# Kernel optimization log

Measured on AMD Instinct MI355X. Metric: run time of the kernel, lower is better.

## Reference

```python
import jax, jax.numpy as jnp
import numpy as np

T_HORIZON, S_DIM, A_DIM, H = 65536, 128, 8, 256
GAMMA, LMBDA, EPS_CLIP, VF_COEF, ENT_COEF = 0.99, 0.95, 0.2, 0.5, 0.01
LOG2PI = float(np.log(2.0 * np.pi))


def setup_inputs() -> dict:
    key = jax.random.key(0)
    ks = jax.random.split(key, 24)
    s = jax.random.normal(ks[0], (T_HORIZON, S_DIM), jnp.float32)
    a = jax.random.normal(ks[1], (T_HORIZON, A_DIM), jnp.float32)
    r = jax.random.normal(ks[2], (T_HORIZON, 1), jnp.float32)
    sp = jax.random.normal(ks[3], (T_HORIZON, S_DIM), jnp.float32)
    log_prob_a_old = jax.random.normal(ks[4], (T_HORIZON, 1), jnp.float32)
    d_mask = (jax.random.uniform(ks[5], (T_HORIZON, 1)) > 0.05).astype(jnp.float32)

    def lin(k, fan_in, fan_out, std):
        return jax.random.normal(k, (fan_in, fan_out), jnp.float32) * (std / np.sqrt(fan_in))

    params = dict(
        pi_W1=lin(ks[6], S_DIM, H, np.sqrt(2)), pi_b1=jnp.zeros((H,), jnp.float32),
        pi_W2=lin(ks[7], H, H, np.sqrt(2)),     pi_b2=jnp.zeros((H,), jnp.float32),
        mu_W=lin(ks[8], H, A_DIM, 0.01),        mu_b=jnp.zeros((A_DIM,), jnp.float32),
        log_std=jnp.zeros((A_DIM,), jnp.float32),
        v_W1=lin(ks[9], S_DIM, H, np.sqrt(2)),  v_b1=jnp.zeros((H,), jnp.float32),
        v_W2=lin(ks[10], H, H, np.sqrt(2)),     v_b2=jnp.zeros((H,), jnp.float32),
        vh_W=lin(ks[11], H, 1, 1.0),            vh_b=jnp.zeros((1,), jnp.float32),
    )
    return dict(s=s, a=a, r=r, sp=sp, log_prob_a_old=log_prob_a_old, d_mask=d_mask, **params)


def reference(s, a, r, sp, log_prob_a_old, d_mask,
              pi_W1, pi_b1, pi_W2, pi_b2, mu_W, mu_b, log_std,
              v_W1, v_b1, v_W2, v_b2, vh_W, vh_b):
    def mlp(x, W1, b1, W2, b2):
        return jnp.tanh(jnp.tanh(x @ W1 + b1) @ W2 + b2)

    def v_fn(x):
        return mlp(x, v_W1, v_b1, v_W2, v_b2) @ vh_W + vh_b  # [N, 1]

    # ---- GAE (computed under no_grad in the original) ----
    values = jax.lax.stop_gradient(v_fn(s))                  # [T, 1]
    v_last = jax.lax.stop_gradient(v_fn(sp[-1:]))            # [1, 1]
    next_values = jnp.concatenate([values[1:], v_last], axis=0)
    deltas = r + GAMMA * next_values * d_mask - values       # [T, 1]

    def gae_step(gae, inp):
        delta, m = inp
        gae = delta + GAMMA * LMBDA * m * gae
        return gae, gae

    _, advantages = jax.lax.scan(gae_step, jnp.zeros((1,), deltas.dtype),
                                 (deltas, d_mask), reverse=True)  # [T, 1]
    returns = advantages + values
    advantages = (advantages - advantages.mean()) / (advantages.std(ddof=1) + 1e-8)
    advantages = jax.lax.stop_gradient(advantages)
    returns = jax.lax.stop_gradient(returns)

    # ---- PPO clipped loss (single full-batch pass) ----
    mu = mlp(s, pi_W1, pi_b1, pi_W2, pi_b2) @ mu_W + mu_b    # [T, A]
    std = jnp.exp(log_std)
    log_prob = (-0.5 * ((a - mu) / std) ** 2 - log_std - 0.5 * LOG2PI).sum(-1, keepdims=True)
    ratio = jnp.exp(log_prob - log_prob_a_old)               # [T, 1]
    pg_loss = -jnp.minimum(ratio * advantages,
                           jnp.clip(ratio, 1.0 - EPS_CLIP, 1.0 + EPS_CLIP) * advantages).mean()
    diff = v_fn(s) - returns
    vf_loss = jnp.where(jnp.abs(diff) < 1.0, 0.5 * diff ** 2, jnp.abs(diff) - 0.5).mean()
    entropy = (0.5 + 0.5 * LOG2PI + log_std).mean()          # Normal entropy, constant over batch
    return pg_loss + VF_COEF * vf_loss - ENT_COEF * entropy
```

## Files before the change

kernel.cpp:

```cpp
#include <hip/hip_runtime.h>
#include <math.h>

#define TH 65536
#define SD 128
#define AD 8
#define HD 256

constexpr float GAMMA  = 0.99f;
constexpr float LMBDA  = 0.95f;
constexpr float EPSC   = 0.2f;
constexpr float VFC    = 0.5f;
constexpr float ENTC   = 0.01f;
constexpr float LOG2PI = 1.8378770664093453f;

typedef _Float16 half8 __attribute__((ext_vector_type(8)));
typedef __fp16 fp16x2 __attribute__((ext_vector_type(2)));
typedef __attribute__((ext_vector_type(4))) float f32x4;

constexpr size_t WS_VALUES = 0;
constexpr size_t WS_RATIO  = 131080;
constexpr size_t WS_CHP    = 196616;
constexpr size_t WS_CHB    = 196680;
constexpr size_t WS_SCAL   = 196744;
constexpr size_t WS_BF     = 196752;
constexpr size_t SW_PIW1 = 0;
constexpr size_t SW_PIW2 = 32768;
constexpr size_t SW_VW1  = 98304;
constexpr size_t SW_VW2  = 131072;
constexpr size_t WS_S1P  = 295056;
constexpr size_t WS_S2P  = 295120;
constexpr size_t WS_VFP  = 295184;
constexpr size_t WS_PGP  = 295248;

__device__ __forceinline__ unsigned pk2h(float a, float b) {
    fp16x2 h = __builtin_amdgcn_cvt_pkrtz(a, b);
    return __builtin_bit_cast(unsigned, h);
}

__device__ __forceinline__ float ftanh(float x) {
    float e = __expf(x + x);
    return fmaf(-2.f, __builtin_amdgcn_rcpf(e + 1.f), 1.f);
}

__device__ __forceinline__ float atomLoad(const float* p) {
    return __hip_atomic_load(p, __ATOMIC_RELAXED, __HIP_MEMORY_SCOPE_AGENT);
}

__global__ __launch_bounds__(256) void swizzle_kernel(
    const float* __restrict__ piW1, const float* __restrict__ vW1,
    const float* __restrict__ piW2, const float* __restrict__ vW2,
    unsigned short* __restrict__ dPiW1, unsigned short* __restrict__ dVW1,
    unsigned short* __restrict__ dPiW2, unsigned short* __restrict__ dVW2,
    float* __restrict__ scal)
{
    if (blockIdx.x == 0 && threadIdx.x < 8) scal[threadIdx.x] = 0.f;
    int g = blockIdx.x * 256 + threadIdx.x;
    const float* S; unsigned short* D; int lo;
    if      (g <  8192) { S = piW1; D = dPiW1; lo = 0;     }
    else if (g < 24576) { S = piW2; D = dPiW2; lo = 8192;  }
    else if (g < 32768) { S = vW1;  D = dVW1;  lo = 24576; }
    else                { S = vW2;  D = dVW2;  lo = 32768; }
    int q = g - lo;
    int k = q >> 6, n4 = (q & 63) * 4;
    float4 v = *(const float4*)(S + (size_t)k * HD + n4);
    int ks = k >> 5, kq = (k >> 3) & 3, j = k & 7;
    int nt = n4 >> 4, nr = n4 & 15;
    unsigned short* base = D + ((size_t)(ks * 16 + nt) * 64 + kq * 16 + nr) * 8 + j;
    unsigned p01 = pk2h(v.x, v.y);
    unsigned p23 = pk2h(v.z, v.w);
    base[0]  = (unsigned short)(p01 & 0xffff);
    base[8]  = (unsigned short)(p01 >> 16);
    base[16] = (unsigned short)(p23 & 0xffff);
    base[24] = (unsigned short)(p23 >> 16);
}

__device__ __forceinline__ void runlayer1(
    f32x4* acc, const unsigned short* __restrict__ Ws,
    const half8* afr, int colhalf, int lane)
{
    const half8* Wp = (const half8*)Ws + (size_t)(colhalf * 8) * 64 + lane;
    half8 b[2][8];
#pragma unroll
    for (int nt = 0; nt < 8; ++nt) acc[nt] = (f32x4){0.f, 0.f, 0.f, 0.f};
#pragma unroll
    for (int nt = 0; nt < 8; ++nt) b[0][nt] = Wp[(0 * 16 + nt) * 64];
#pragma unroll
    for (int nt = 0; nt < 8; ++nt) b[1][nt] = Wp[(1 * 16 + nt) * 64];
#pragma unroll
    for (int ks = 0; ks < 4; ++ks) {
        const int cur = ks & 1;
#pragma unroll
        for (int nt = 0; nt < 8; ++nt)
            acc[nt] = __builtin_amdgcn_mfma_f32_16x16x32_f16(afr[ks], b[cur][nt], acc[nt], 0, 0, 0);
        if (ks < 2) {
#pragma unroll
            for (int nt = 0; nt < 8; ++nt) b[cur][nt] = Wp[((ks + 2) * 16 + nt) * 64];
        }
    }
}

__device__ __forceinline__ void runlayer2(
    f32x4* acc, const unsigned short* __restrict__ Ws,
    const unsigned short* h1, int l15, int quad, int rowgrp, int colhalf, int lane)
{
    const half8* Wp = (const half8*)Ws + (size_t)(colhalf * 8) * 64 + lane;
    const unsigned short* Ap = h1 + (rowgrp * 16 + l15) * 264 + quad * 8;
    half8 b[2][8];
    half8 af[2];
#pragma unroll
    for (int nt = 0; nt < 8; ++nt) acc[nt] = (f32x4){0.f, 0.f, 0.f, 0.f};
    af[0] = *(const half8*)(Ap + 0 * 32);
#pragma unroll
    for (int nt = 0; nt < 8; ++nt) b[0][nt] = Wp[(0 * 16 + nt) * 64];
    af[1] = *(const half8*)(Ap + 1 * 32);
#pragma unroll
    for (int nt = 0; nt < 8; ++nt) b[1][nt] = Wp[(1 * 16 + nt) * 64];
#pragma unroll
    for (int ks = 0; ks < 8; ++ks) {
        const int cur = ks & 1;
#pragma unroll
        for (int nt = 0; nt < 8; ++nt)
            acc[nt] = __builtin_amdgcn_mfma_f32_16x16x32_f16(af[cur], b[cur][nt], acc[nt], 0, 0, 0);
        if (ks < 6) {
            af[cur] = *(const half8*)(Ap + (ks + 2) * 32);
#pragma unroll
            for (int nt = 0; nt < 8; ++nt) b[cur][nt] = Wp[((ks + 2) * 16 + nt) * 64];
        }
    }
}

__device__ __forceinline__ void store4(unsigned short* dst, int stride,
                                       float t0, float t1, float t2, float t3)
{
    unsigned p01 = pk2h(t0, t1), p23 = pk2h(t2, t3);
    dst[0]          = (unsigned short)(p01 & 0xffff);
    dst[stride]     = (unsigned short)(p01 >> 16);
    dst[2 * stride] = (unsigned short)(p23 & 0xffff);
    dst[3 * stride] = (unsigned short)(p23 >> 16);
}

__global__ __launch_bounds__(256, 3) void mlp_fused_kernel(
    const float* __restrict__ X, const float* __restrict__ Xlast,
    const unsigned short* __restrict__ piW1s, const float* __restrict__ pib1,
    const unsigned short* __restrict__ piW2s, const float* __restrict__ pib2,
    const float* __restrict__ muW, const float* __restrict__ mub,
    const float* __restrict__ logstd,
    const float* __restrict__ act, const float* __restrict__ lpold,
    const unsigned short* __restrict__ vW1s, const float* __restrict__ vb1,
    const unsigned short* __restrict__ vW2s, const float* __restrict__ vb2,
    const float* __restrict__ vhW, const float* __restrict__ vhb,
    float* __restrict__ values, float* __restrict__ ratio)
{
    __shared__ unsigned short h1[32 * 264];
    __shared__ float cmb[32 * 8];
    __shared__ float val[32];
    const int tid = threadIdx.x;
    const int lane = tid & 63, wave = tid >> 6;
    const int l15 = lane & 15, quad = lane >> 4;
    const int rowgrp = wave >> 1, colhalf = wave & 1;
    const bool vonly = (blockIdx.x == gridDim.x - 1);
    const float* Xp = vonly ? Xlast : X + (size_t)blockIdx.x * 32 * SD;
    const int nrows = vonly ? 1 : 32;
    const int vout0 = vonly ? TH : blockIdx.x * 32;

    if (tid < 32) val[tid] = 0.f;
    cmb[tid] = 0.f;

    const int rr = rowgrp * 16 + l15;
    const float* xrow = Xp + (size_t)(rr < nrows ? rr : 0) * SD;
    half8 afr[4];
#pragma unroll
    for (int ks = 0; ks < 4; ++ks) {
        float4 v0 = *(const float4*)(xrow + ks * 32 + quad * 8);
        float4 v1 = *(const float4*)(xrow + ks * 32 + quad * 8 + 4);
        if (rr >= nrows) { v0 = make_float4(0.f, 0.f, 0.f, 0.f); v1 = v0; }
        uint4 u = make_uint4(pk2h(v0.x, v0.y), pk2h(v0.z, v0.w),
                             pk2h(v1.x, v1.y), pk2h(v1.z, v1.w));
        afr[ks] = __builtin_bit_cast(half8, u);
    }

    f32x4 acc[8];

    if (!vonly) {
        runlayer1(acc, piW1s, afr, colhalf, lane);
#pragma unroll
        for (int ntl = 0; ntl < 8; ++ntl) {
            int col = (colhalf * 8 + ntl) * 16 + l15;
            float bb = pib1[col];
            store4(&h1[(rowgrp * 16 + quad * 4) * 264 + col], 264,
                   ftanh(acc[ntl][0] + bb), ftanh(acc[ntl][1] + bb),
                   ftanh(acc[ntl][2] + bb), ftanh(acc[ntl][3] + bb));
        }
        __syncthreads();
        runlayer2(acc, piW2s, h1, l15, quad, rowgrp, colhalf, lane);
        float pm[4][8];
#pragma unroll
        for (int rg = 0; rg < 4; ++rg)
#pragma unroll
            for (int aj = 0; aj < 8; ++aj) pm[rg][aj] = 0.f;
#pragma unroll
        for (int ntl = 0; ntl < 8; ++ntl) {
            int col = (colhalf * 8 + ntl) * 16 + l15;
            float bb = pib2[col];
            float4 w0 = *(const float4*)(muW + (size_t)col * AD);
            float4 w1 = *(const float4*)(muW + (size_t)col * AD + 4);
            float wv[8] = {w0.x, w0.y, w0.z, w0.w, w1.x, w1.y, w1.z, w1.w};
#pragma unroll
            for (int rg = 0; rg < 4; ++rg) {
                float hv = ftanh(acc[ntl][rg] + bb);
#pragma unroll
                for (int aj = 0; aj < 8; ++aj) pm[rg][aj] = fmaf(hv, wv[aj], pm[rg][aj]);
            }
        }
#pragma unroll
        for (int off = 8; off >= 1; off >>= 1)
#pragma unroll
            for (int rg = 0; rg < 4; ++rg)
#pragma unroll
                for (int aj = 0; aj < 8; ++aj)
                    pm[rg][aj] += __shfl_xor(pm[rg][aj], off, 16);
        if (l15 == 0) {
#pragma unroll
            for (int rg = 0; rg < 4; ++rg) {
                int rowi = rowgrp * 16 + quad * 4 + rg;
#pragma unroll
                for (int aj = 0; aj < 8; ++aj)
                    atomicAdd(&cmb[rowi * 8 + aj], pm[rg][aj]);
            }
        }
        __syncthreads();
        if (tid < 32) {
            int row = blockIdx.x * 32 + tid;
            const float* ar = act + (size_t)row * AD;
            float lp = 0.f;
#pragma unroll
            for (int aj = 0; aj < 8; ++aj) {
                float ls = logstd[aj];
                float mu = cmb[tid * 8 + aj] + mub[aj];
                float z = (ar[aj] - mu) * __expf(-ls);
                lp += -0.5f * z * z - ls;
            }
            lp -= 4.f * LOG2PI;
            ratio[row] = __expf(lp - lpold[row]);
        }
        __syncthreads();
    }

    runlayer1(acc, vW1s, afr, colhalf, lane);
#pragma unroll
    for (int ntl = 0; ntl < 8; ++ntl) {
        int col = (colhalf * 8 + ntl) * 16 + l15;
        float bb = vb1[col];
        store4(&h1[(rowgrp * 16 + quad * 4) * 264 + col], 264,
               ftanh(acc[ntl][0] + bb), ftanh(acc[ntl][1] + bb),
               ftanh(acc[ntl][2] + bb), ftanh(acc[ntl][3] + bb));
    }
    __syncthreads();
    runlayer2(acc, vW2s, h1, l15, quad, rowgrp, colhalf, lane);
    float vp[4] = {0.f, 0.f, 0.f, 0.f};
#pragma unroll
    for (int ntl = 0; ntl < 8; ++ntl) {
        int col = (colhalf * 8 + ntl) * 16 + l15;
        float bb = vb2[col], w = vhW[col];
#pragma unroll
        for (int rg = 0; rg < 4; ++rg) vp[rg] += ftanh(acc[ntl][rg] + bb) * w;
    }
#pragma unroll
    for (int off = 8; off >= 1; off >>= 1)
#pragma unroll
        for (int rg = 0; rg < 4; ++rg) vp[rg] += __shfl_xor(vp[rg], off, 16);
    if (l15 == 0) {
#pragma unroll
        for (int rg = 0; rg < 4; ++rg)
            atomicAdd(&val[rowgrp * 16 + quad * 4 + rg], vp[rg]);
    }
    __syncthreads();
    if (tid < nrows)
        values[vout0 + tid] = val[tid] + vhb[0];
}

__device__ __forceinline__ void gae_block_scan(
    const float* __restrict__ rw, const float* __restrict__ m,
    const float* __restrict__ values, int t0, int j,
    float* sp_, float* sb_, float* ds, float* ms)
{
    float4 vv = *(const float4*)(values + t0);
    float v4 = values[t0 + 4];
    float4 rr = *(const float4*)(rw + t0);
    float4 mm = *(const float4*)(m + t0);
    float vs[5] = {vv.x, vv.y, vv.z, vv.w, v4};
    float rs[4] = {rr.x, rr.y, rr.z, rr.w};
    ms[0] = mm.x; ms[1] = mm.y; ms[2] = mm.z; ms[3] = mm.w;
    const float g = GAMMA * LMBDA;
#pragma unroll
    for (int i = 0; i < 4; ++i)
        ds[i] = rs[i] + GAMMA * vs[i + 1] * ms[i] - vs[i];

    float P = 1.f, B = 0.f;
#pragma unroll
    for (int i = 3; i >= 0; --i) {
        float p = g * ms[i];
        B = ds[i] + p * B;
        P = p * P;
    }
    sp_[j] = P; sb_[j] = B;
    __syncthreads();
    for (int dstep = 1; dstep < 256; dstep <<= 1) {
        float pj = sp_[j], bj = sb_[j], pk = 1.f, bk = 0.f;
        if (j + dstep < 256) { pk = sp_[j + dstep]; bk = sb_[j + dstep]; }
        __syncthreads();
        sp_[j] = pj * pk;
        sb_[j] = bj + pj * bk;
        __syncthreads();
    }
}

__device__ __forceinline__ float gae_carry(
    const float* __restrict__ chunkP, const float* __restrict__ chunkB,
    int j, int bid, float* cp, float* cb, float* bcast)
{
    if (j < 64) { cp[j] = chunkP[j]; cb[j] = chunkB[j]; }
    __syncthreads();
    if (j == 0) {
        float A = 0.f;
        for (int c = 63; c > bid; --c) A = cb[c] + cp[c] * A;
        bcast[0] = A;
    }
    __syncthreads();
    return bcast[0];
}

__global__ __launch_bounds__(256) void gae_scan_kernel(
    const float* __restrict__ rw, const float* __restrict__ m,
    const float* __restrict__ values,
    float* __restrict__ chunkP, float* __restrict__ chunkB)
{
    __shared__ float sp_[256], sb_[256];
    const int j = threadIdx.x;
    float ds[4], ms[4];
    gae_block_scan(rw, m, values, blockIdx.x * 1024 + j * 4, j, sp_, sb_, ds, ms);
    if (j == 0) { chunkP[blockIdx.x] = sp_[0]; chunkB[blockIdx.x] = sb_[0]; }
}

__global__ __launch_bounds__(256) void gae_mid_kernel(
    const float* __restrict__ rw, const float* __restrict__ m,
    const float* __restrict__ values,
    const float* __restrict__ chunkP, const float* __restrict__ chunkB,
    float* __restrict__ s1p, float* __restrict__ s2p, float* __restrict__ vfp)
{
    __shared__ float sp_[256], sb_[256];
    __shared__ float cp[64], cb[64];
    __shared__ float red[12];
    __shared__ float bcast[1];
    const int j = threadIdx.x;
    const float g = GAMMA * LMBDA;
    float ds[4], ms[4];
    gae_block_scan(rw, m, values, blockIdx.x * 1024 + j * 4, j, sp_, sb_, ds, ms);
    const float carry = gae_carry(chunkP, chunkB, j, blockIdx.x, cp, cb, bcast);

    float Pe = 1.f, Be = 0.f;
    if (j < 255) { Pe = sp_[j + 1]; Be = sb_[j + 1]; }
    float A = Be + Pe * carry;
    float s1 = 0.f, s2 = 0.f, vf = 0.f;
#pragma unroll
    for (int i = 3; i >= 0; --i) {
        A = ds[i] + g * ms[i] * A;
        float ab = fabsf(A);
        vf += (ab < 1.f) ? 0.5f * A * A : ab - 0.5f;
        s1 += A;
        s2 += A * A;
    }
#pragma unroll
    for (int off = 32; off >= 1; off >>= 1) {
        s1 += __shfl_down(s1, off, 64);
        s2 += __shfl_down(s2, off, 64);
        vf += __shfl_down(vf, off, 64);
    }
    if ((j & 63) == 0) {
        int w = j >> 6;
        red[w] = s1; red[4 + w] = s2; red[8 + w] = vf;
    }
    __syncthreads();
    if (j == 0) {
        s1p[blockIdx.x] = red[0] + red[1] + red[2] + red[3];
        s2p[blockIdx.x] = red[4] + red[5] + red[6] + red[7];
        vfp[blockIdx.x] = red[8] + red[9] + red[10] + red[11];
    }
}

__global__ __launch_bounds__(256) void gae_fin_kernel(
    const float* __restrict__ rw, const float* __restrict__ m,
    const float* __restrict__ values, const float* __restrict__ ratio,
    const float* __restrict__ logstd,
    const float* __restrict__ chunkP, const float* __restrict__ chunkB,
    const float* __restrict__ s1p, const float* __restrict__ s2p,
    const float* __restrict__ vfp,
    float* __restrict__ pgp, float* __restrict__ scal, float* __restrict__ out)
{
    __shared__ float sp_[256], sb_[256];
    __shared__ float cp[64], cb[64];
    __shared__ float red[4];
    __shared__ float bcast[4];
    const int j = threadIdx.x;
    const int t0 = blockIdx.x * 1024 + j * 4;
    const float g = GAMMA * LMBDA;
    float ds[4], ms[4];
    gae_block_scan(rw, m, values, t0, j, sp_, sb_, ds, ms);
    const float carry = gae_carry(chunkP, chunkB, j, blockIdx.x, cp, cb, bcast);

    if (j < 64) {
        float a = s1p[j], b = s2p[j], c = vfp[j];
#pragma unroll
        for (int off = 32; off >= 1; off >>= 1) {
            a += __shfl_down(a, off, 64);
            b += __shfl_down(b, off, 64);
            c += __shfl_down(c, off, 64);
        }
        if (j == 0) { bcast[1] = a; bcast[2] = b; bcast[3] = c; }
    }
    __syncthreads();
    const float ssum = bcast[1], ssq = bcast[2], vfs = bcast[3];
    const float meanA = ssum / (float)TH;
    const float varA = fmaxf((ssq - ssum * ssum / (float)TH) / (float)(TH - 1), 0.f);
    const float inv = 1.f / (sqrtf(varA) + 1e-8f);

    float Pe = 1.f, Be = 0.f;
    if (j < 255) { Pe = sp_[j + 1]; Be = sb_[j + 1]; }
    float A = Be + Pe * carry;
    float a4[4];
#pragma unroll
    for (int i = 3; i >= 0; --i) {
        A = ds[i] + g * ms[i] * A;
        a4[i] = A;
    }

    float4 r4 = *(const float4*)(ratio + t0);
    float rt[4] = {r4.x, r4.y, r4.z, r4.w};
    float pg = 0.f;
#pragma unroll
    for (int i = 0; i < 4; ++i) {
        float aN = (a4[i] - meanA) * inv;
        float rc = fminf(fmaxf(rt[i], 1.f - EPSC), 1.f + EPSC);
        pg -= fminf(rt[i] * aN, rc * aN);
    }
#pragma unroll
    for (int off = 32; off >= 1; off >>= 1) pg += __shfl_down(pg, off, 64);
    if ((j & 63) == 0) red[j >> 6] = pg;
    __syncthreads();
    if (j == 0) {
        pgp[blockIdx.x] = red[0] + red[1] + red[2] + red[3];
        __threadfence();
        float old = atomicAdd(&scal[4], 1.f);
        if (old == 63.f) {
            float pgs = 0.f;
            for (int c = 0; c < 64; ++c) pgs += atomLoad(&pgp[c]);
            float ls = 0.f;
#pragma unroll
            for (int jj = 0; jj < AD; ++jj) ls += logstd[jj];
            float entropy = 0.5f + 0.5f * LOG2PI + ls / (float)AD;
            out[0] = pgs / (float)TH + VFC * (vfs / (float)TH) - ENTC * entropy;
        }
    }
}

extern "C" void kernel_launch(void* const* d_in, const int* in_sizes, int n_in,
                              void* d_out, int out_size, void* d_ws, size_t ws_size,
                              hipStream_t stream) {
    const float* s      = (const float*)d_in[0];
    const float* a      = (const float*)d_in[1];
    const float* r      = (const float*)d_in[2];
    const float* sp     = (const float*)d_in[3];
    const float* lpold  = (const float*)d_in[4];
    const float* dmask  = (const float*)d_in[5];
    const float* piW1   = (const float*)d_in[6];
    const float* pib1   = (const float*)d_in[7];
    const float* piW2   = (const float*)d_in[8];
    const float* pib2   = (const float*)d_in[9];
    const float* muW    = (const float*)d_in[10];
    const float* mub    = (const float*)d_in[11];
    const float* logstd = (const float*)d_in[12];
    const float* vW1    = (const float*)d_in[13];
    const float* vb1    = (const float*)d_in[14];
    const float* vW2    = (const float*)d_in[15];
    const float* vb2    = (const float*)d_in[16];
    const float* vhW    = (const float*)d_in[17];
    const float* vhb    = (const float*)d_in[18];

    float* ws      = (float*)d_ws;
    float* values  = ws + WS_VALUES;
    float* ratio   = ws + WS_RATIO;
    float* chunkP  = ws + WS_CHP;
    float* chunkB  = ws + WS_CHB;
    float* scal    = ws + WS_SCAL;
    float* s1p     = ws + WS_S1P;
    float* s2p     = ws + WS_S2P;
    float* vfp     = ws + WS_VFP;
    float* pgp     = ws + WS_PGP;
    unsigned short* bfbase = (unsigned short*)(ws + WS_BF);
    unsigned short* dPiW1 = bfbase + SW_PIW1;
    unsigned short* dPiW2 = bfbase + SW_PIW2;
    unsigned short* dVW1  = bfbase + SW_VW1;
    unsigned short* dVW2  = bfbase + SW_VW2;

    swizzle_kernel<<<192, 256, 0, stream>>>(piW1, vW1, piW2, vW2,
                                            dPiW1, dVW1, dPiW2, dVW2, scal);

    mlp_fused_kernel<<<TH / 32 + 1, 256, 0, stream>>>(
        s, sp + (size_t)(TH - 1) * SD,
        dPiW1, pib1, dPiW2, pib2, muW, mub, logstd, a, lpold,
        dVW1, vb1, dVW2, vb2, vhW, vhb,
        values, ratio);

    gae_scan_kernel<<<64, 256, 0, stream>>>(r, dmask, values, chunkP, chunkB);
    gae_mid_kernel<<<64, 256, 0, stream>>>(r, dmask, values, chunkP, chunkB,
                                           s1p, s2p, vfp);
    gae_fin_kernel<<<64, 256, 0, stream>>>(r, dmask, values, ratio, logstd,
                                           chunkP, chunkB, s1p, s2p, vfp,
                                           pgp, scal, (float*)d_out);
}
```

Before: 211.5 us.

## Stage MLP weight chunks into LDS with async global_load_lds double buffering

Replaces per-wave direct global loads of the swizzled fp16 weights with cooperative asynchronous global-to-LDS copies into a double-buffered 32 KB shared buffer. The next K-chunk, or the first chunk of the next layer, is prefetched while MFMAs consume the current one. Each chunk is loaded once per block instead of once by each of the two row-group waves, which halves global/L2 weight traffic and frees registers. In exchange it adds a __syncthreads per K-step and more LDS use, which may reduce occupancy. There is no explicit vmcnt wait before the barrier, so correctness depends on the barrier ordering the asynchronous copies.

```diff
diff --git a/kernel.cpp b/kernel.cpp
--- a/kernel.cpp
+++ b/kernel.cpp
@@ -44,6 +44,22 @@
 
 __device__ __forceinline__ float atomLoad(const float* p) {
     return __hip_atomic_load(p, __ATOMIC_RELAXED, __HIP_MEMORY_SCOPE_AGENT);
+}
+
+__device__ __forceinline__ void stage_chunk(
+    const unsigned short* __restrict__ W, int ks,
+    unsigned short* lbuf, int wave, int lane)
+{
+    const char* src = (const char*)W + (size_t)ks * 16384
+                    + (size_t)wave * 4096 + (size_t)lane * 16;
+    char* dst = (char*)lbuf + wave * 4096;
+#pragma unroll
+    for (int f = 0; f < 4; ++f) {
+        __builtin_amdgcn_global_load_lds(
+            (const __attribute__((address_space(1))) void*)(src + f * 1024),
+            (__attribute__((address_space(3))) void*)(dst + f * 1024),
+            16, 0, 0);
+    }
 }
 
 __global__ __launch_bounds__(256) void swizzle_kernel(
@@ -74,61 +90,6 @@
     base[24] = (unsigned short)(p23 >> 16);
 }
 
-__device__ __forceinline__ void runlayer1(
-    f32x4* acc, const unsigned short* __restrict__ Ws,
-    const half8* afr, int colhalf, int lane)
-{
-    const half8* Wp = (const half8*)Ws + (size_t)(colhalf * 8) * 64 + lane;
-    half8 b[2][8];
-#pragma unroll
-    for (int nt = 0; nt < 8; ++nt) acc[nt] = (f32x4){0.f, 0.f, 0.f, 0.f};
-#pragma unroll
-    for (int nt = 0; nt < 8; ++nt) b[0][nt] = Wp[(0 * 16 + nt) * 64];
-#pragma unroll
-    for (int nt = 0; nt < 8; ++nt) b[1][nt] = Wp[(1 * 16 + nt) * 64];
-#pragma unroll
-    for (int ks = 0; ks < 4; ++ks) {
-        const int cur = ks & 1;
-#pragma unroll
-        for (int nt = 0; nt < 8; ++nt)
-            acc[nt] = __builtin_amdgcn_mfma_f32_16x16x32_f16(afr[ks], b[cur][nt], acc[nt], 0, 0, 0);
-        if (ks < 2) {
-#pragma unroll
-            for (int nt = 0; nt < 8; ++nt) b[cur][nt] = Wp[((ks + 2) * 16 + nt) * 64];
-        }
-    }
-}
-
-__device__ __forceinline__ void runlayer2(
-    f32x4* acc, const unsigned short* __restrict__ Ws,
-    const unsigned short* h1, int l15, int quad, int rowgrp, int colhalf, int lane)
-{
-    const half8* Wp = (const half8*)Ws + (size_t)(colhalf * 8) * 64 + lane;
-    const unsigned short* Ap = h1 + (rowgrp * 16 + l15) * 264 + quad * 8;
-    half8 b[2][8];
-    half8 af[2];
-#pragma unroll
-    for (int nt = 0; nt < 8; ++nt) acc[nt] = (f32x4){0.f, 0.f, 0.f, 0.f};
-    af[0] = *(const half8*)(Ap + 0 * 32);
-#pragma unroll
-    for (int nt = 0; nt < 8; ++nt) b[0][nt] = Wp[(0 * 16 + nt) * 64];
-    af[1] = *(const half8*)(Ap + 1 * 32);
-#pragma unroll
-    for (int nt = 0; nt < 8; ++nt) b[1][nt] = Wp[(1 * 16 + nt) * 64];
-#pragma unroll
-    for (int ks = 0; ks < 8; ++ks) {
-        const int cur = ks & 1;
-#pragma unroll
-        for (int nt = 0; nt < 8; ++nt)
-            acc[nt] = __builtin_amdgcn_mfma_f32_16x16x32_f16(af[cur], b[cur][nt], acc[nt], 0, 0, 0);
-        if (ks < 6) {
-            af[cur] = *(const half8*)(Ap + (ks + 2) * 32);
-#pragma unroll
-            for (int nt = 0; nt < 8; ++nt) b[cur][nt] = Wp[((ks + 2) * 16 + nt) * 64];
-        }
-    }
-}
-
 __device__ __forceinline__ void store4(unsigned short* dst, int stride,
                                        float t0, float t1, float t2, float t3)
 {
@@ -151,7 +112,8 @@
     const float* __restrict__ vhW, const float* __restrict__ vhb,
     float* __restrict__ values, float* __restrict__ ratio)
 {
-    __shared__ unsigned short h1[32 * 264];
+    __shared__ __align__(16) unsigned short wbuf[2][8192];
+    __shared__ __align__(16) unsigned short h1[32 * 264];
     __shared__ float cmb[32 * 8];
     __shared__ float val[32];
     const int tid = threadIdx.x;
@@ -166,6 +128,8 @@
     if (tid < 32) val[tid] = 0.f;
     cmb[tid] = 0.f;
 
+    stage_chunk(vonly ? vW1s : piW1s, 0, wbuf[0], wave, lane);
+
     const int rr = rowgrp * 16 + l15;
     const float* xrow = Xp + (size_t)(rr < nrows ? rr : 0) * SD;
     half8 afr[4];
@@ -180,9 +144,22 @@
     }
 
     f32x4 acc[8];
+    __syncthreads();
 
     if (!vonly) {
-        runlayer1(acc, piW1s, afr, colhalf, lane);
+#pragma unroll
+        for (int nt = 0; nt < 8; ++nt) acc[nt] = (f32x4){0.f, 0.f, 0.f, 0.f};
+#pragma unroll
+        for (int ks = 0; ks < 4; ++ks) {
+            if (ks < 3) stage_chunk(piW1s, ks + 1, wbuf[(ks + 1) & 1], wave, lane);
+            else        stage_chunk(piW2s, 0, wbuf[0], wave, lane);
+            const half8* bb = (const half8*)wbuf[ks & 1];
+#pragma unroll
+            for (int ntl = 0; ntl < 8; ++ntl)
+                acc[ntl] = __builtin_amdgcn_mfma_f32_16x16x32_f16(
+                    afr[ks], bb[(colhalf * 8 + ntl) * 64 + lane], acc[ntl], 0, 0, 0);
+            __syncthreads();
+        }
 #pragma unroll
         for (int ntl = 0; ntl < 8; ++ntl) {
             int col = (colhalf * 8 + ntl) * 16 + l15;
@@ -192,7 +169,23 @@
                    ftanh(acc[ntl][2] + bb), ftanh(acc[ntl][3] + bb));
         }
         __syncthreads();
-        runlayer2(acc, piW2s, h1, l15, quad, rowgrp, colhalf, lane);
+#pragma unroll
+        for (int nt = 0; nt < 8; ++nt) acc[nt] = (f32x4){0.f, 0.f, 0.f, 0.f};
+        {
+            const unsigned short* Ap = h1 + (rowgrp * 16 + l15) * 264 + quad * 8;
+#pragma unroll
+            for (int ks = 0; ks < 8; ++ks) {
+                if (ks < 7) stage_chunk(piW2s, ks + 1, wbuf[(ks + 1) & 1], wave, lane);
+                else        stage_chunk(vW1s, 0, wbuf[0], wave, lane);
+                half8 af = *(const half8*)(Ap + ks * 32);
+                const half8* bb = (const half8*)wbuf[ks & 1];
+#pragma unroll
+                for (int ntl = 0; ntl < 8; ++ntl)
+                    acc[ntl] = __builtin_amdgcn_mfma_f32_16x16x32_f16(
+                        af, bb[(colhalf * 8 + ntl) * 64 + lane], acc[ntl], 0, 0, 0);
+                __syncthreads();
+            }
+        }
         float pm[4][8];
 #pragma unroll
         for (int rg = 0; rg < 4; ++rg)
@@ -246,7 +239,19 @@
         __syncthreads();
     }
 
-    runlayer1(acc, vW1s, afr, colhalf, lane);
+#pragma unroll
+    for (int nt = 0; nt < 8; ++nt) acc[nt] = (f32x4){0.f, 0.f, 0.f, 0.f};
+#pragma unroll
+    for (int ks = 0; ks < 4; ++ks) {
+        if (ks < 3) stage_chunk(vW1s, ks + 1, wbuf[(ks + 1) & 1], wave, lane);
+        else        stage_chunk(vW2s, 0, wbuf[0], wave, lane);
+        const half8* bb = (const half8*)wbuf[ks & 1];
+#pragma unroll
+        for (int ntl = 0; ntl < 8; ++ntl)
+            acc[ntl] = __builtin_amdgcn_mfma_f32_16x16x32_f16(
+                afr[ks], bb[(colhalf * 8 + ntl) * 64 + lane], acc[ntl], 0, 0, 0);
+        __syncthreads();
+    }
 #pragma unroll
     for (int ntl = 0; ntl < 8; ++ntl) {
         int col = (colhalf * 8 + ntl) * 16 + l15;
@@ -256,7 +261,22 @@
                ftanh(acc[ntl][2] + bb), ftanh(acc[ntl][3] + bb));
     }
     __syncthreads();
-    runlayer2(acc, vW2s, h1, l15, quad, rowgrp, colhalf, lane);
+#pragma unroll
+    for (int nt = 0; nt < 8; ++nt) acc[nt] = (f32x4){0.f, 0.f, 0.f, 0.f};
+    {
+        const unsigned short* Ap = h1 + (rowgrp * 16 + l15) * 264 + quad * 8;
+#pragma unroll
+        for (int ks = 0; ks < 8; ++ks) {
+            if (ks < 7) stage_chunk(vW2s, ks + 1, wbuf[(ks + 1) & 1], wave, lane);
+            half8 af = *(const half8*)(Ap + ks * 32);
+            const half8* bb = (const half8*)wbuf[ks & 1];
+#pragma unroll
+            for (int ntl = 0; ntl < 8; ++ntl)
+                acc[ntl] = __builtin_amdgcn_mfma_f32_16x16x32_f16(
+                    af, bb[(colhalf * 8 + ntl) * 64 + lane], acc[ntl], 0, 0, 0);
+            __syncthreads();
+        }
+    }
     float vp[4] = {0.f, 0.f, 0.f, 0.f};
 #pragma unroll
     for (int ntl = 0; ntl < 8; ++ntl) {
```

After: 215.1 us. Within noise of the previous version (+1.7%).
